# Kernel optimization log

Hardware: AMD Instinct MI355X
Metric: run time of the kernel (lower is better)

## Reference

```python
import jax, jax.numpy as jnp
import numpy as np

NUM_EXPERTS = 8
TOP_K = 2
HIDDEN = 512
INTER = 2048
BALANCE_COEF = 0.01


def setup_inputs() -> dict:
    key = jax.random.key(0)
    ks = jax.random.split(key, 5)
    B, S = 2, 1024
    scale_in = 1.0 / np.sqrt(HIDDEN)
    scale_mid = 1.0 / np.sqrt(INTER)
    return {
        "hidden_states": jax.random.normal(ks[0], (B, S, HIDDEN), jnp.float32),
        "w_router": jax.random.normal(ks[1], (HIDDEN, NUM_EXPERTS), jnp.float32) * scale_in,
        "b_router": jnp.zeros((NUM_EXPERTS,), jnp.float32),
        "w1": jax.random.normal(ks[2], (NUM_EXPERTS, HIDDEN, INTER), jnp.float32) * scale_in,
        "b1": jnp.zeros((NUM_EXPERTS, INTER), jnp.float32),
        "w2": jax.random.normal(ks[3], (NUM_EXPERTS, INTER, HIDDEN), jnp.float32) * scale_mid,
        "b2": jnp.zeros((NUM_EXPERTS, HIDDEN), jnp.float32),
    }


def reference(hidden_states, w_router, b_router, w1, b1, w2, b2):
    B, S, H = hidden_states.shape
    E, K = NUM_EXPERTS, TOP_K

    # ---- Router: softmax over experts, top-k selection, renormalized weights ----
    logits = jnp.einsum("bsh,he->bse", hidden_states, w_router) + b_router  # (B,S,E)
    probs = jax.nn.softmax(logits, axis=-1)
    top_vals, top_idx = jax.lax.top_k(probs, K)                              # (B,S,K)
    routing_weights = top_vals / jnp.sum(top_vals, axis=-1, keepdims=True)   # renorm to sum 1

    # ---- Load-balancing auxiliary loss: coef * E * sum_e f_e * P_e ----
    assign = jax.nn.one_hot(top_idx, E, dtype=probs.dtype)                   # (B,S,K,E)
    f = jnp.mean(assign, axis=(0, 1, 2))                                     # fraction routed per expert
    P = jnp.mean(probs, axis=(0, 1))                                         # mean router prob per expert
    balance_loss = BALANCE_COEF * E * jnp.sum(f * P)

    # ---- Phase 1: flatten (B,S,H) -> (B*S*K, H) token-slots ----
    T = B * S * K
    tokens_flat = jnp.broadcast_to(hidden_states[:, :, None, :], (B, S, K, H)).reshape(T, H)
    weights_flat = routing_weights.reshape(T)
    experts_flat = top_idx.reshape(T)

    # ---- Phase 2: per-expert MLP, masked combine ----
    out_flat = jnp.zeros_like(tokens_flat)
    for e in range(E):
        hmid = jax.nn.gelu(tokens_flat @ w1[e] + b1[e])                      # (T, INTER)
        y = hmid @ w2[e] + b2[e]                                             # (T, H)
        mask = (experts_flat == e)
        out_flat = out_flat + jnp.where(mask[:, None], y * weights_flat[:, None], 0.0)

    # ---- Phase 3: combine over K and residual ----
    combined = out_flat.reshape(B, S, K, H).sum(axis=2)
    output = combined + hidden_states
    return output, balance_loss
```

## Files before the change

kernel.cpp:

```cpp
#include <hip/hip_runtime.h>
#include <math.h>

#define NT 2048
#define TSLOTS 4096
#define HID 512
#define INTER 2048
#define NE 8
#define TM 64
#define BKG 64
#define MAXTILES 72
#define PSLOTS 4608

#define WS_HMID      0
#define WS_PROBS     0
#define WS_TOPIDX    65536
#define WS_TOPW      81920
#define WS_TILE_E    18874368
#define WS_TILE_B    18874880
#define WS_TILE_V    18875392
#define WS_PERM      18875904
#define WS_PW        18894336
#define WS_ISLOT     18912768
#define WS_XB        18929152
#define WS_WT        21026304
#define WS_Y         37803520

typedef __attribute__((ext_vector_type(8))) short bf16x8;
typedef __attribute__((ext_vector_type(4))) float f32x4;
typedef __attribute__((ext_vector_type(8))) unsigned short ushort8;

__device__ __forceinline__ unsigned short f2bf(float f) {
    union { float f; unsigned u; } v; v.f = f;
    unsigned r = v.u + 0x7FFF + ((v.u >> 16) & 1);
    return (unsigned short)(r >> 16);
}
__device__ __forceinline__ float bf2f(unsigned short b) {
    union { unsigned u; float f; } v; v.u = ((unsigned)b) << 16;
    return v.f;
}

__device__ __forceinline__ void gload16(const void* g, void* l) {
    __builtin_amdgcn_global_load_lds(
        (const __attribute__((address_space(1))) unsigned int*)g,
        (__attribute__((address_space(3))) unsigned int*)l, 16, 0, 0);
}

__device__ __forceinline__ float gelu_fast(float x) {
    float t = 1.5957691f * x + 0.0713548f * x * x * x;
    return x / (1.0f + __expf(-t));
}

__global__ __launch_bounds__(64) void route_k(
    const float* __restrict__ hs, const float* __restrict__ wr,
    const float* __restrict__ br,
    unsigned short* __restrict__ xb,
    float* __restrict__ probs, int* __restrict__ topidx, float* __restrict__ topw)
{
    int t = blockIdx.x;
    int lane = threadIdx.x;
    const float* x = hs + (size_t)t * HID + lane * 8;
    float4 v0 = *(const float4*)x;
    float4 v1 = *(const float4*)(x + 4);

    ushort8 ob;
    ob[0] = f2bf(v0.x); ob[1] = f2bf(v0.y); ob[2] = f2bf(v0.z); ob[3] = f2bf(v0.w);
    ob[4] = f2bf(v1.x); ob[5] = f2bf(v1.y); ob[6] = f2bf(v1.z); ob[7] = f2bf(v1.w);
    *(ushort8*)(xb + (size_t)t * HID + lane * 8) = ob;

    float xv[8] = {v0.x, v0.y, v0.z, v0.w, v1.x, v1.y, v1.z, v1.w};
    float acc[NE];
#pragma unroll
    for (int e = 0; e < NE; e++) acc[e] = 0.0f;
    const float* w = wr + (size_t)lane * 8 * NE;
#pragma unroll
    for (int j = 0; j < 8; j++) {
        float4 wa = *(const float4*)(w + j * NE);
        float4 wb = *(const float4*)(w + j * NE + 4);
        acc[0] += xv[j] * wa.x; acc[1] += xv[j] * wa.y;
        acc[2] += xv[j] * wa.z; acc[3] += xv[j] * wa.w;
        acc[4] += xv[j] * wb.x; acc[5] += xv[j] * wb.y;
        acc[6] += xv[j] * wb.z; acc[7] += xv[j] * wb.w;
    }
#pragma unroll
    for (int off = 32; off > 0; off >>= 1) {
#pragma unroll
        for (int e = 0; e < NE; e++) acc[e] += __shfl_down(acc[e], off);
    }
    if (lane == 0) {
        float l[NE], p[NE];
        float m = -1e30f;
#pragma unroll
        for (int e = 0; e < NE; e++) { l[e] = acc[e] + br[e]; m = fmaxf(m, l[e]); }
        float s = 0.0f;
#pragma unroll
        for (int e = 0; e < NE; e++) { p[e] = expf(l[e] - m); s += p[e]; }
        float inv = 1.0f / s;
#pragma unroll
        for (int e = 0; e < NE; e++) { p[e] *= inv; probs[(size_t)t * NE + e] = p[e]; }
        int i1 = 0;
#pragma unroll
        for (int e = 1; e < NE; e++) if (p[e] > p[i1]) i1 = e;
        int i2 = (i1 == 0) ? 1 : 0;
#pragma unroll
        for (int e = 0; e < NE; e++) if (e != i1 && p[e] > p[i2]) i2 = e;
        float denom = 1.0f / (p[i1] + p[i2]);
        topidx[2 * t]     = i1;
        topidx[2 * t + 1] = i2;
        topw[2 * t]       = p[i1] * denom;
        topw[2 * t + 1]   = p[i2] * denom;
    }
}

__global__ __launch_bounds__(256) void plan_k(
    const float* __restrict__ probs, const int* __restrict__ topidx,
    const float* __restrict__ topw,
    int* __restrict__ tile_e, int* __restrict__ tile_b, int* __restrict__ tile_v,
    int* __restrict__ perm, float* __restrict__ pw, int* __restrict__ islot,
    float* __restrict__ loss_out)
{
    int tid = threadIdx.x;
    int lane = tid & 63, wave = tid >> 6;

    float ps[NE];
    int c[NE];
#pragma unroll
    for (int e = 0; e < NE; e++) { ps[e] = 0.0f; c[e] = 0; }
    for (int t = tid; t < NT; t += 256) {
        float4 p0 = *(const float4*)&probs[(size_t)t * NE];
        float4 p1 = *(const float4*)&probs[(size_t)t * NE + 4];
        ps[0] += p0.x; ps[1] += p0.y; ps[2] += p0.z; ps[3] += p0.w;
        ps[4] += p1.x; ps[5] += p1.y; ps[6] += p1.z; ps[7] += p1.w;
    }
    for (int t = tid; t < TSLOTS; t += 256) c[topidx[t]]++;
#pragma unroll
    for (int off = 32; off > 0; off >>= 1) {
#pragma unroll
        for (int e = 0; e < NE; e++) {
            ps[e] += __shfl_down(ps[e], off);
            c[e]  += __shfl_down(c[e], off);
        }
    }
    __shared__ float sps[4][NE];
    __shared__ int sc[4][NE];
    __shared__ int scur[NE];
    if (lane == 0) {
#pragma unroll
        for (int e = 0; e < NE; e++) { sps[wave][e] = ps[e]; sc[wave][e] = c[e]; }
    }
    __syncthreads();
    if (tid == 0) {
        float loss = 0.0f;
        int b = 0, tidx = 0;
        for (int e = 0; e < NE; e++) {
            float pse = sps[0][e] + sps[1][e] + sps[2][e] + sps[3][e];
            int ce = sc[0][e] + sc[1][e] + sc[2][e] + sc[3][e];
            loss += ((float)ce / (float)TSLOTS) * (pse / (float)NT);
            int nt = (ce + TM - 1) / TM;
            scur[e] = b;
            for (int i = 0; i < nt; i++) {
                tile_e[tidx] = e;
                tile_b[tidx] = b + i * TM;
                int v = ce - i * TM;
                tile_v[tidx] = v > TM ? TM : v;
                tidx++;
            }
            b += nt * TM;
        }
        for (; tidx < MAXTILES; tidx++) tile_e[tidx] = -1;
        loss_out[0] = 0.01f * (float)NE * loss;
    }
    __syncthreads();
    for (int t = tid; t < TSLOTS; t += 256) {
        int e = topidx[t];
        int p = atomicAdd(&scur[e], 1);
        perm[p] = t;
        pw[p] = topw[t];
        islot[t] = p;
    }
}

__global__ __launch_bounds__(256) void convT_k(const float* __restrict__ src,
                                               unsigned short* __restrict__ dst,
                                               int K, int N)
{
    int e = blockIdx.z;
    int n0 = blockIdx.x * 32, k0 = blockIdx.y * 32;
    const float* s = src + (size_t)e * K * N;
    unsigned short* d = dst + (size_t)e * N * K;
    __shared__ float T[32][33];
    int tid = threadIdx.x;
    int r = tid >> 3, c4 = (tid & 7) * 4;
    float4 v = *(const float4*)(s + (size_t)(k0 + r) * N + n0 + c4);
    T[r][c4 + 0] = v.x; T[r][c4 + 1] = v.y; T[r][c4 + 2] = v.z; T[r][c4 + 3] = v.w;
    __syncthreads();
    ushort4 o;
    o.x = f2bf(T[c4 + 0][r]); o.y = f2bf(T[c4 + 1][r]);
    o.z = f2bf(T[c4 + 2][r]); o.w = f2bf(T[c4 + 3][r]);
    *(ushort4*)(d + (size_t)(n0 + r) * K + k0 + c4) = o;
}

__global__ __launch_bounds__(256) void gemm1_k(
    const unsigned short* __restrict__ xb, const unsigned short* __restrict__ w1t,
    const float* __restrict__ b1,
    const int* __restrict__ tile_e, const int* __restrict__ tile_b,
    const int* __restrict__ tile_v, const int* __restrict__ perm,
    unsigned short* __restrict__ hmid)
{
    int tt = blockIdx.y;
    int e = tile_e[tt];
    if (e < 0) return;
    int p0 = tile_b[tt], nv = tile_v[tt];
    int n0 = blockIdx.x * 128;

    __shared__ unsigned short As[64 * 64];
    __shared__ unsigned short Bs[128 * 64];

    int tid = threadIdx.x;
    int lane = tid & 63, wave = tid >> 6;
    int wm = (wave >> 1) * 32, wn = (wave & 1) * 64;

    int rA = tid >> 3, gs = tid & 7;
    int rA2 = rA + 32;
    int tokA = perm[p0 + ((rA < nv) ? rA : 0)] >> 1;
    int tokA2 = perm[p0 + ((rA2 < nv) ? rA2 : 0)] >> 1;
    const unsigned short* apt1 = xb + (size_t)tokA * HID + (gs ^ (rA & 7)) * 8;
    const unsigned short* apt2 = xb + (size_t)tokA2 * HID + (gs ^ (rA2 & 7)) * 8;
    const unsigned short* bbase = w1t + (size_t)e * INTER * HID;
    const unsigned short* bpt0 = bbase + (size_t)(n0 + rA) * HID + (gs ^ (rA & 7)) * 8;
    const unsigned short* bpt1 = bbase + (size_t)(n0 + rA + 32) * HID + (gs ^ ((rA + 32) & 7)) * 8;
    const unsigned short* bpt2 = bbase + (size_t)(n0 + rA + 64) * HID + (gs ^ ((rA + 64) & 7)) * 8;
    const unsigned short* bpt3 = bbase + (size_t)(n0 + rA + 96) * HID + (gs ^ ((rA + 96) & 7)) * 8;

    f32x4 acc[2][4] = {};
    int fm = lane & 15, fq = lane >> 4;

    for (int k0 = 0; k0 < HID; k0 += BKG) {
        __syncthreads();
        gload16(apt1 + k0, (void*)(As + tid * 8));
        gload16(apt2 + k0, (void*)(As + 2048 + tid * 8));
        gload16(bpt0 + k0, (void*)(Bs + tid * 8));
        gload16(bpt1 + k0, (void*)(Bs + 2048 + tid * 8));
        gload16(bpt2 + k0, (void*)(Bs + 4096 + tid * 8));
        gload16(bpt3 + k0, (void*)(Bs + 6144 + tid * 8));
        __syncthreads();
#pragma unroll
        for (int kk = 0; kk < 2; kk++) {
            bf16x8 af[2], bfr[4];
#pragma unroll
            for (int mt = 0; mt < 2; mt++) {
                int R = wm + mt * 16 + fm;
                int G = (kk * 4 + fq) ^ (R & 7);
                af[mt] = *(const bf16x8*)&As[R * 64 + G * 8];
            }
#pragma unroll
            for (int nt = 0; nt < 4; nt++) {
                int R = wn + nt * 16 + fm;
                int G = (kk * 4 + fq) ^ (R & 7);
                bfr[nt] = *(const bf16x8*)&Bs[R * 64 + G * 8];
            }
#pragma unroll
            for (int mt = 0; mt < 2; mt++)
#pragma unroll
                for (int nt = 0; nt < 4; nt++)
                    acc[mt][nt] = __builtin_amdgcn_mfma_f32_16x16x32_bf16(
                        af[mt], bfr[nt], acc[mt][nt], 0, 0, 0);
        }
    }

    int cn = lane & 15, crb = (lane >> 4) * 4;
#pragma unroll
    for (int mt = 0; mt < 2; mt++) {
#pragma unroll
        for (int r = 0; r < 4; r++) {
            int m = wm + mt * 16 + crb + r;
            size_t rowoff = (size_t)(p0 + m) * INTER;
#pragma unroll
            for (int nt = 0; nt < 4; nt++) {
                int gn = n0 + wn + nt * 16 + cn;
                float vv = acc[mt][nt][r] + b1[e * INTER + gn];
                hmid[rowoff + gn] = f2bf(gelu_fast(vv));
            }
        }
    }
}

__global__ __launch_bounds__(256) void gemm2_k(
    const unsigned short* __restrict__ hmid, const unsigned short* __restrict__ w2t,
    const float* __restrict__ b2,
    const int* __restrict__ tile_e, const int* __restrict__ tile_b,
    unsigned short* __restrict__ y)
{
    int tt = blockIdx.y;
    int e = tile_e[tt];
    if (e < 0) return;
    int p0 = tile_b[tt];
    int n0 = blockIdx.x * 64;
    int kz = blockIdx.z;
    int kbeg = kz * (INTER / 2), kend = kbeg + INTER / 2;
    unsigned short* yk = y + (size_t)kz * PSLOTS * HID;

    __shared__ unsigned short As[64 * 64];
    __shared__ unsigned short Bs[64 * 64];

    int tid = threadIdx.x;
    int lane = tid & 63, wave = tid >> 6;
    int wm = (wave >> 1) * 32, wn = (wave & 1) * 32;

    int rA = tid >> 3, gs = tid & 7;
    int rA2 = rA + 32;
    const unsigned short* apt1 = hmid + (size_t)(p0 + rA) * INTER + (gs ^ (rA & 7)) * 8;
    const unsigned short* apt2 = hmid + (size_t)(p0 + rA2) * INTER + (gs ^ (rA2 & 7)) * 8;
    const unsigned short* bbase = w2t + (size_t)e * HID * INTER;
    const unsigned short* bpt1 = bbase + (size_t)(n0 + rA) * INTER + (gs ^ (rA & 7)) * 8;
    const unsigned short* bpt2 = bbase + (size_t)(n0 + rA2) * INTER + (gs ^ (rA2 & 7)) * 8;

    f32x4 acc[2][2] = {};
    int fm = lane & 15, fq = lane >> 4;

    for (int k0 = kbeg; k0 < kend; k0 += BKG) {
        __syncthreads();
        gload16(apt1 + k0, (void*)(As + tid * 8));
        gload16(apt2 + k0, (void*)(As + 2048 + tid * 8));
        gload16(bpt1 + k0, (void*)(Bs + tid * 8));
        gload16(bpt2 + k0, (void*)(Bs + 2048 + tid * 8));
        __syncthreads();
#pragma unroll
        for (int kk = 0; kk < 2; kk++) {
            bf16x8 af[2], bfr[2];
#pragma unroll
            for (int mt = 0; mt < 2; mt++) {
                int R = wm + mt * 16 + fm;
                int G = (kk * 4 + fq) ^ (R & 7);
                af[mt] = *(const bf16x8*)&As[R * 64 + G * 8];
            }
#pragma unroll
            for (int nt = 0; nt < 2; nt++) {
                int R = wn + nt * 16 + fm;
                int G = (kk * 4 + fq) ^ (R & 7);
                bfr[nt] = *(const bf16x8*)&Bs[R * 64 + G * 8];
            }
#pragma unroll
            for (int mt = 0; mt < 2; mt++)
#pragma unroll
                for (int nt = 0; nt < 2; nt++)
                    acc[mt][nt] = __builtin_amdgcn_mfma_f32_16x16x32_bf16(
                        af[mt], bfr[nt], acc[mt][nt], 0, 0, 0);
        }
    }

    int cn = lane & 15, crb = (lane >> 4) * 4;
#pragma unroll
    for (int mt = 0; mt < 2; mt++) {
#pragma unroll
        for (int r = 0; r < 4; r++) {
            int m = wm + mt * 16 + crb + r;
            size_t rowoff = (size_t)(p0 + m) * HID;
#pragma unroll
            for (int nt = 0; nt < 2; nt++) {
                int gn = n0 + wn + nt * 16 + cn;
                float bias = (kz == 0) ? b2[e * HID + gn] : 0.0f;
                yk[rowoff + gn] = f2bf(acc[mt][nt][r] + bias);
            }
        }
    }
}

__global__ __launch_bounds__(64) void combine_k(
    const float* __restrict__ hs, const unsigned short* __restrict__ y,
    const int* __restrict__ islot, const float* __restrict__ pw,
    float* __restrict__ out)
{
    int t = blockIdx.x;
    int lane = threadIdx.x;
    int pA = islot[2 * t], pB = islot[2 * t + 1];
    float wA = pw[pA], wB = pw[pB];
    int c = lane * 8;
    const unsigned short* yA0 = y + (size_t)pA * HID + c;
    const unsigned short* yB0 = y + (size_t)pB * HID + c;
    const unsigned short* yA1 = yA0 + (size_t)PSLOTS * HID;
    const unsigned short* yB1 = yB0 + (size_t)PSLOTS * HID;
    ushort8 a0 = *(const ushort8*)yA0;
    ushort8 a1 = *(const ushort8*)yA1;
    ushort8 b0 = *(const ushort8*)yB0;
    ushort8 b1 = *(const ushort8*)yB1;
    const float* h = hs + (size_t)t * HID + c;
    float4 h0 = *(const float4*)h;
    float4 h1 = *(const float4*)(h + 4);
    float o[8];
#pragma unroll
    for (int j = 0; j < 8; j++)
        o[j] = wA * (bf2f(a0[j]) + bf2f(a1[j])) + wB * (bf2f(b0[j]) + bf2f(b1[j]));
    float4 r0 = {o[0] + h0.x, o[1] + h0.y, o[2] + h0.z, o[3] + h0.w};
    float4 r1 = {o[4] + h1.x, o[5] + h1.y, o[6] + h1.z, o[7] + h1.w};
    float* op = out + (size_t)t * HID + c;
    *(float4*)op = r0;
    *(float4*)(op + 4) = r1;
}

extern "C" void kernel_launch(void* const* d_in, const int* in_sizes, int n_in,
                              void* d_out, int out_size, void* d_ws, size_t ws_size,
                              hipStream_t stream) {
    const float* hs = (const float*)d_in[0];
    const float* wr = (const float*)d_in[1];
    const float* br = (const float*)d_in[2];
    const float* w1 = (const float*)d_in[3];
    const float* b1 = (const float*)d_in[4];
    const float* w2 = (const float*)d_in[5];
    const float* b2 = (const float*)d_in[6];
    float* out = (float*)d_out;

    char* ws = (char*)d_ws;
    float* probs           = (float*)(ws + WS_PROBS);
    int*   topidx          = (int*)(ws + WS_TOPIDX);
    float* topw            = (float*)(ws + WS_TOPW);
    int*   tile_e          = (int*)(ws + WS_TILE_E);
    int*   tile_b          = (int*)(ws + WS_TILE_B);
    int*   tile_v          = (int*)(ws + WS_TILE_V);
    int*   perm            = (int*)(ws + WS_PERM);
    float* pw              = (float*)(ws + WS_PW);
    int*   islot           = (int*)(ws + WS_ISLOT);
    unsigned short* xb     = (unsigned short*)(ws + WS_XB);
    unsigned short* wt     = (unsigned short*)(ws + WS_WT);
    unsigned short* hmid   = (unsigned short*)(ws + WS_HMID);
    unsigned short* y      = (unsigned short*)(ws + WS_Y);

    route_k<<<NT, 64, 0, stream>>>(hs, wr, br, xb, probs, topidx, topw);
    plan_k<<<1, 256, 0, stream>>>(probs, topidx, topw, tile_e, tile_b, tile_v,
                                  perm, pw, islot, out + (size_t)NT * HID);
    convT_k<<<dim3(INTER / 32, HID / 32, NE), 256, 0, stream>>>(w1, wt, HID, INTER);
    gemm1_k<<<dim3(INTER / 128, MAXTILES), 256, 0, stream>>>(
        xb, wt, b1, tile_e, tile_b, tile_v, perm, hmid);
    convT_k<<<dim3(HID / 32, INTER / 32, NE), 256, 0, stream>>>(w2, wt, INTER, HID);
    gemm2_k<<<dim3(HID / 64, MAXTILES, 2), 256, 0, stream>>>(
        hmid, wt, b2, tile_e, tile_b, y);
    combine_k<<<NT, 64, 0, stream>>>(hs, y, islot, pw, out);
}
```

Measured before the change: 193.0 us.

## Fuse routing and weight transposes into one kernel, vectorize GEMM epilogues

Routing and both weight transpose/bf16-convert passes now run in a single pre-kernel launch, using separate workspace buffers for w1t and w2t so the two transposes no longer serialize around gemm1. Plan tile generation is parallelized across threads. The GEMM MFMA operands are swapped so each lane owns 4 consecutive output columns, allowing float4 bias loads and ushort4 stores in the epilogues. Combine packs 4 tokens per 256-thread block. This trades extra workspace memory for fewer launches and more coalesced epilogue writes.

```diff
diff --git a/kernel.cpp b/kernel.cpp
--- a/kernel.cpp
+++ b/kernel.cpp
@@ -10,6 +10,7 @@
 #define BKG 64
 #define MAXTILES 72
 #define PSLOTS 4608
+#define ROUTE_BLOCKS 512
 
 #define WS_HMID      0
 #define WS_PROBS     0
@@ -22,8 +23,9 @@
 #define WS_PW        18894336
 #define WS_ISLOT     18912768
 #define WS_XB        18929152
-#define WS_WT        21026304
-#define WS_Y         37803520
+#define WS_W1T       21026304
+#define WS_W2T       37803520
+#define WS_Y         54580736
 
 typedef __attribute__((ext_vector_type(8))) short bf16x8;
 typedef __attribute__((ext_vector_type(4))) float f32x4;
@@ -50,65 +52,101 @@
     return x / (1.0f + __expf(-t));
 }
 
-__global__ __launch_bounds__(64) void route_k(
+__global__ __launch_bounds__(256) void pre_k(
     const float* __restrict__ hs, const float* __restrict__ wr,
     const float* __restrict__ br,
+    const float* __restrict__ w1, const float* __restrict__ w2,
     unsigned short* __restrict__ xb,
+    unsigned short* __restrict__ w1t, unsigned short* __restrict__ w2t,
     float* __restrict__ probs, int* __restrict__ topidx, float* __restrict__ topw)
 {
-    int t = blockIdx.x;
-    int lane = threadIdx.x;
-    const float* x = hs + (size_t)t * HID + lane * 8;
-    float4 v0 = *(const float4*)x;
-    float4 v1 = *(const float4*)(x + 4);
-
-    ushort8 ob;
-    ob[0] = f2bf(v0.x); ob[1] = f2bf(v0.y); ob[2] = f2bf(v0.z); ob[3] = f2bf(v0.w);
-    ob[4] = f2bf(v1.x); ob[5] = f2bf(v1.y); ob[6] = f2bf(v1.z); ob[7] = f2bf(v1.w);
-    *(ushort8*)(xb + (size_t)t * HID + lane * 8) = ob;
-
-    float xv[8] = {v0.x, v0.y, v0.z, v0.w, v1.x, v1.y, v1.z, v1.w};
-    float acc[NE];
-#pragma unroll
-    for (int e = 0; e < NE; e++) acc[e] = 0.0f;
-    const float* w = wr + (size_t)lane * 8 * NE;
-#pragma unroll
-    for (int j = 0; j < 8; j++) {
-        float4 wa = *(const float4*)(w + j * NE);
-        float4 wb = *(const float4*)(w + j * NE + 4);
-        acc[0] += xv[j] * wa.x; acc[1] += xv[j] * wa.y;
-        acc[2] += xv[j] * wa.z; acc[3] += xv[j] * wa.w;
-        acc[4] += xv[j] * wb.x; acc[5] += xv[j] * wb.y;
-        acc[6] += xv[j] * wb.z; acc[7] += xv[j] * wb.w;
-    }
-#pragma unroll
-    for (int off = 32; off > 0; off >>= 1) {
-#pragma unroll
-        for (int e = 0; e < NE; e++) acc[e] += __shfl_down(acc[e], off);
-    }
-    if (lane == 0) {
-        float l[NE], p[NE];
-        float m = -1e30f;
-#pragma unroll
-        for (int e = 0; e < NE; e++) { l[e] = acc[e] + br[e]; m = fmaxf(m, l[e]); }
-        float s = 0.0f;
-#pragma unroll
-        for (int e = 0; e < NE; e++) { p[e] = expf(l[e] - m); s += p[e]; }
-        float inv = 1.0f / s;
-#pragma unroll
-        for (int e = 0; e < NE; e++) { p[e] *= inv; probs[(size_t)t * NE + e] = p[e]; }
-        int i1 = 0;
-#pragma unroll
-        for (int e = 1; e < NE; e++) if (p[e] > p[i1]) i1 = e;
-        int i2 = (i1 == 0) ? 1 : 0;
-#pragma unroll
-        for (int e = 0; e < NE; e++) if (e != i1 && p[e] > p[i2]) i2 = e;
-        float denom = 1.0f / (p[i1] + p[i2]);
-        topidx[2 * t]     = i1;
-        topidx[2 * t + 1] = i2;
-        topw[2 * t]       = p[i1] * denom;
-        topw[2 * t + 1]   = p[i2] * denom;
-    }
+    __shared__ float T[32][33];
+    int bx = blockIdx.x;
+    int tid = threadIdx.x;
+
+    if (bx < ROUTE_BLOCKS) {
+        int lane = tid & 63, wave = tid >> 6;
+        int t = bx * 4 + wave;
+        const float* x = hs + (size_t)t * HID + lane * 8;
+        float4 v0 = *(const float4*)x;
+        float4 v1 = *(const float4*)(x + 4);
+
+        ushort8 ob;
+        ob[0] = f2bf(v0.x); ob[1] = f2bf(v0.y); ob[2] = f2bf(v0.z); ob[3] = f2bf(v0.w);
+        ob[4] = f2bf(v1.x); ob[5] = f2bf(v1.y); ob[6] = f2bf(v1.z); ob[7] = f2bf(v1.w);
+        *(ushort8*)(xb + (size_t)t * HID + lane * 8) = ob;
+
+        float xv[8] = {v0.x, v0.y, v0.z, v0.w, v1.x, v1.y, v1.z, v1.w};
+        float acc[NE];
+#pragma unroll
+        for (int e = 0; e < NE; e++) acc[e] = 0.0f;
+        const float* w = wr + (size_t)lane * 8 * NE;
+#pragma unroll
+        for (int j = 0; j < 8; j++) {
+            float4 wa = *(const float4*)(w + j * NE);
+            float4 wb = *(const float4*)(w + j * NE + 4);
+            acc[0] += xv[j] * wa.x; acc[1] += xv[j] * wa.y;
+            acc[2] += xv[j] * wa.z; acc[3] += xv[j] * wa.w;
+            acc[4] += xv[j] * wb.x; acc[5] += xv[j] * wb.y;
+            acc[6] += xv[j] * wb.z; acc[7] += xv[j] * wb.w;
+        }
+#pragma unroll
+        for (int off = 32; off > 0; off >>= 1) {
+#pragma unroll
+            for (int e = 0; e < NE; e++) acc[e] += __shfl_down(acc[e], off);
+        }
+        if (lane == 0) {
+            float l[NE], p[NE];
+            float m = -1e30f;
+#pragma unroll
+            for (int e = 0; e < NE; e++) { l[e] = acc[e] + br[e]; m = fmaxf(m, l[e]); }
+            float s = 0.0f;
+#pragma unroll
+            for (int e = 0; e < NE; e++) { p[e] = expf(l[e] - m); s += p[e]; }
+            float inv = 1.0f / s;
+#pragma unroll
+            for (int e = 0; e < NE; e++) { p[e] *= inv; probs[(size_t)t * NE + e] = p[e]; }
+            int i1 = 0;
+#pragma unroll
+            for (int e = 1; e < NE; e++) if (p[e] > p[i1]) i1 = e;
+            int i2 = (i1 == 0) ? 1 : 0;
+#pragma unroll
+            for (int e = 0; e < NE; e++) if (e != i1 && p[e] > p[i2]) i2 = e;
+            float denom = 1.0f / (p[i1] + p[i2]);
+            topidx[2 * t]     = i1;
+            topidx[2 * t + 1] = i2;
+            topw[2 * t]       = p[i1] * denom;
+            topw[2 * t + 1]   = p[i2] * denom;
+        }
+        return;
+    }
+
+    int t = bx - ROUTE_BLOCKS;
+    const float* src;
+    unsigned short* dst;
+    int K, N, n0, k0;
+    if (t < 8192) {
+        int e = t >> 10, rem = t & 1023;
+        n0 = (rem & 63) * 32; k0 = (rem >> 6) * 32;
+        src = w1 + (size_t)e * HID * INTER;
+        dst = w1t + (size_t)e * INTER * HID;
+        K = HID; N = INTER;
+    } else {
+        t -= 8192;
+        int e = t >> 10, rem = t & 1023;
+        n0 = (rem & 15) * 32; k0 = (rem >> 4) * 32;
+        src = w2 + (size_t)e * INTER * HID;
+        dst = w2t + (size_t)e * HID * INTER;
+        K = INTER; N = HID;
+    }
+    int r = tid >> 3, c4 = (tid & 7) * 4;
+    float4 v = *(const float4*)(src + (size_t)(k0 + r) * N + n0 + c4);
+    T[r][c4 + 0] = v.x; T[r][c4 + 1] = v.y; T[r][c4 + 2] = v.z; T[r][c4 + 3] = v.w;
+    __syncthreads();
+    ushort4 o;
+    o.x = f2bf(T[c4 + 0][r]); o.y = f2bf(T[c4 + 1][r]);
+    o.z = f2bf(T[c4 + 2][r]); o.w = f2bf(T[c4 + 3][r]);
+    *(ushort4*)(dst + (size_t)(n0 + r) * K + k0 + c4) = o;
 }
 
 __global__ __launch_bounds__(256) void plan_k(
@@ -142,7 +180,7 @@
     }
     __shared__ float sps[4][NE];
     __shared__ int sc[4][NE];
-    __shared__ int scur[NE];
+    __shared__ int scur[NE], sbase[NE], scnt[NE], spref[NE + 1];
     if (lane == 0) {
 #pragma unroll
         for (int e = 0; e < NE; e++) { sps[wave][e] = ps[e]; sc[wave][e] = c[e]; }
@@ -150,24 +188,29 @@
     __syncthreads();
     if (tid == 0) {
         float loss = 0.0f;
-        int b = 0, tidx = 0;
+        int b = 0, tp = 0;
         for (int e = 0; e < NE; e++) {
             float pse = sps[0][e] + sps[1][e] + sps[2][e] + sps[3][e];
             int ce = sc[0][e] + sc[1][e] + sc[2][e] + sc[3][e];
             loss += ((float)ce / (float)TSLOTS) * (pse / (float)NT);
             int nt = (ce + TM - 1) / TM;
-            scur[e] = b;
-            for (int i = 0; i < nt; i++) {
-                tile_e[tidx] = e;
-                tile_b[tidx] = b + i * TM;
-                int v = ce - i * TM;
-                tile_v[tidx] = v > TM ? TM : v;
-                tidx++;
-            }
+            sbase[e] = b; scnt[e] = ce; scur[e] = b; spref[e] = tp;
+            tp += nt;
             b += nt * TM;
         }
-        for (; tidx < MAXTILES; tidx++) tile_e[tidx] = -1;
+        spref[NE] = tp;
         loss_out[0] = 0.01f * (float)NE * loss;
+    }
+    __syncthreads();
+    for (int tx = tid; tx < MAXTILES; tx += 256) {
+        if (tx >= spref[NE]) { tile_e[tx] = -1; continue; }
+        int e = 0;
+        while (tx >= spref[e + 1]) e++;
+        int i = tx - spref[e];
+        tile_e[tx] = e;
+        tile_b[tx] = sbase[e] + i * TM;
+        int v = scnt[e] - i * TM;
+        tile_v[tx] = v > TM ? TM : v;
     }
     __syncthreads();
     for (int t = tid; t < TSLOTS; t += 256) {
@@ -177,26 +220,6 @@
         pw[p] = topw[t];
         islot[t] = p;
     }
-}
-
-__global__ __launch_bounds__(256) void convT_k(const float* __restrict__ src,
-                                               unsigned short* __restrict__ dst,
-                                               int K, int N)
-{
-    int e = blockIdx.z;
-    int n0 = blockIdx.x * 32, k0 = blockIdx.y * 32;
-    const float* s = src + (size_t)e * K * N;
-    unsigned short* d = dst + (size_t)e * N * K;
-    __shared__ float T[32][33];
-    int tid = threadIdx.x;
-    int r = tid >> 3, c4 = (tid & 7) * 4;
-    float4 v = *(const float4*)(s + (size_t)(k0 + r) * N + n0 + c4);
-    T[r][c4 + 0] = v.x; T[r][c4 + 1] = v.y; T[r][c4 + 2] = v.z; T[r][c4 + 3] = v.w;
-    __syncthreads();
-    ushort4 o;
-    o.x = f2bf(T[c4 + 0][r]); o.y = f2bf(T[c4 + 1][r]);
-    o.z = f2bf(T[c4 + 2][r]); o.w = f2bf(T[c4 + 3][r]);
-    *(ushort4*)(d + (size_t)(n0 + r) * K + k0 + c4) = o;
 }
 
 __global__ __launch_bounds__(256) void gemm1_k(
@@ -263,23 +286,25 @@
 #pragma unroll
                 for (int nt = 0; nt < 4; nt++)
                     acc[mt][nt] = __builtin_amdgcn_mfma_f32_16x16x32_bf16(
-                        af[mt], bfr[nt], acc[mt][nt], 0, 0, 0);
-        }
-    }
-
-    int cn = lane & 15, crb = (lane >> 4) * 4;
+                        bfr[nt], af[mt], acc[mt][nt], 0, 0, 0);
+        }
+    }
+
+    int cm = lane & 15, qn = (lane >> 4) * 4;
 #pragma unroll
     for (int mt = 0; mt < 2; mt++) {
-#pragma unroll
-        for (int r = 0; r < 4; r++) {
-            int m = wm + mt * 16 + crb + r;
-            size_t rowoff = (size_t)(p0 + m) * INTER;
-#pragma unroll
-            for (int nt = 0; nt < 4; nt++) {
-                int gn = n0 + wn + nt * 16 + cn;
-                float vv = acc[mt][nt][r] + b1[e * INTER + gn];
-                hmid[rowoff + gn] = f2bf(gelu_fast(vv));
-            }
+        int m = wm + mt * 16 + cm;
+        size_t rowoff = (size_t)(p0 + m) * INTER;
+#pragma unroll
+        for (int nt = 0; nt < 4; nt++) {
+            int nb = n0 + wn + nt * 16 + qn;
+            float4 bb = *(const float4*)(b1 + e * INTER + nb);
+            ushort4 o;
+            o.x = f2bf(gelu_fast(acc[mt][nt][0] + bb.x));
+            o.y = f2bf(gelu_fast(acc[mt][nt][1] + bb.y));
+            o.z = f2bf(gelu_fast(acc[mt][nt][2] + bb.z));
+            o.w = f2bf(gelu_fast(acc[mt][nt][3] + bb.w));
+            *(ushort4*)(hmid + rowoff + nb) = o;
         }
     }
 }
@@ -344,34 +369,38 @@
 #pragma unroll
                 for (int nt = 0; nt < 2; nt++)
                     acc[mt][nt] = __builtin_amdgcn_mfma_f32_16x16x32_bf16(
-                        af[mt], bfr[nt], acc[mt][nt], 0, 0, 0);
-        }
-    }
-
-    int cn = lane & 15, crb = (lane >> 4) * 4;
+                        bfr[nt], af[mt], acc[mt][nt], 0, 0, 0);
+        }
+    }
+
+    int cm = lane & 15, qn = (lane >> 4) * 4;
 #pragma unroll
     for (int mt = 0; mt < 2; mt++) {
-#pragma unroll
-        for (int r = 0; r < 4; r++) {
-            int m = wm + mt * 16 + crb + r;
-            size_t rowoff = (size_t)(p0 + m) * HID;
-#pragma unroll
-            for (int nt = 0; nt < 2; nt++) {
-                int gn = n0 + wn + nt * 16 + cn;
-                float bias = (kz == 0) ? b2[e * HID + gn] : 0.0f;
-                yk[rowoff + gn] = f2bf(acc[mt][nt][r] + bias);
-            }
-        }
-    }
-}
-
-__global__ __launch_bounds__(64) void combine_k(
+        int m = wm + mt * 16 + cm;
+        size_t rowoff = (size_t)(p0 + m) * HID;
+#pragma unroll
+        for (int nt = 0; nt < 2; nt++) {
+            int nb = n0 + wn + nt * 16 + qn;
+            float4 bb = (kz == 0) ? *(const float4*)(b2 + e * HID + nb)
+                                  : float4{0.0f, 0.0f, 0.0f, 0.0f};
+            ushort4 o;
+            o.x = f2bf(acc[mt][nt][0] + bb.x);
+            o.y = f2bf(acc[mt][nt][1] + bb.y);
+            o.z = f2bf(acc[mt][nt][2] + bb.z);
+            o.w = f2bf(acc[mt][nt][3] + bb.w);
+            *(ushort4*)(yk + rowoff + nb) = o;
+        }
+    }
+}
+
+__global__ __launch_bounds__(256) void combine_k(
     const float* __restrict__ hs, const unsigned short* __restrict__ y,
     const int* __restrict__ islot, const float* __restrict__ pw,
     float* __restrict__ out)
 {
-    int t = blockIdx.x;
-    int lane = threadIdx.x;
+    int tid = threadIdx.x;
+    int lane = tid & 63, wave = tid >> 6;
+    int t = blockIdx.x * 4 + wave;
     int pA = islot[2 * t], pB = islot[2 * t + 1];
     float wA = pw[pA], wB = pw[pB];
     int c = lane * 8;
@@ -420,18 +449,18 @@
     float* pw              = (float*)(ws + WS_PW);
     int*   islot           = (int*)(ws + WS_ISLOT);
     unsigned short* xb     = (unsigned short*)(ws + WS_XB);
-    unsigned short* wt     = (unsigned short*)(ws + WS_WT);
+    unsigned short* w1t    = (unsigned short*)(ws + WS_W1T);
+    unsigned short* w2t    = (unsigned short*)(ws + WS_W2T);
     unsigned short* hmid   = (unsigned short*)(ws + WS_HMID);
     unsigned short* y      = (unsigned short*)(ws + WS_Y);
 
-    route_k<<<NT, 64, 0, stream>>>(hs, wr, br, xb, probs, topidx, topw);
+    pre_k<<<ROUTE_BLOCKS + 16384, 256, 0, stream>>>(
+        hs, wr, br, w1, w2, xb, w1t, w2t, probs, topidx, topw);
     plan_k<<<1, 256, 0, stream>>>(probs, topidx, topw, tile_e, tile_b, tile_v,
                                   perm, pw, islot, out + (size_t)NT * HID);
-    convT_k<<<dim3(INTER / 32, HID / 32, NE), 256, 0, stream>>>(w1, wt, HID, INTER);
     gemm1_k<<<dim3(INTER / 128, MAXTILES), 256, 0, stream>>>(
-        xb, wt, b1, tile_e, tile_b, tile_v, perm, hmid);
-    convT_k<<<dim3(HID / 32, INTER / 32, NE), 256, 0, stream>>>(w2, wt, INTER, HID);
+        xb, w1t, b1, tile_e, tile_b, tile_v, perm, hmid);
     gemm2_k<<<dim3(HID / 64, MAXTILES, 2), 256, 0, stream>>>(
-        hmid, wt, b2, tile_e, tile_b, y);
-    combine_k<<<NT, 64, 0, stream>>>(hs, y, islot, pw, out);
-}
+        hmid, w2t, b2, tile_e, tile_b, y);
+    combine_k<<<NT / 4, 256, 0, stream>>>(hs, y, islot, pw, out);
+}
```

Result: no change. 189.7 us (-1.7%).
